# Optimization experiments

Hardware: AMD Instinct MI355X
Metric: run time of the kernel (lower is better)

The kernel has to match this reference:

```python
import jax, jax.numpy as jnp
import numpy as np
from jax import lax

B, S, DIMS, T, K = 4, 4096, 2048, 10, 2


def setup_inputs() -> dict:
    key = jax.random.key(0)
    ks = jax.random.split(key, 4)
    scale = 1.0 / np.sqrt(DIMS)
    x = jax.random.normal(ks[0], (B, S, DIMS), dtype=jnp.float32)
    W_cls = jax.random.normal(ks[1], (DIMS, T), dtype=jnp.float32) * scale
    W_sparse = jax.random.normal(ks[2], (DIMS, T), dtype=jnp.float32) * scale
    W_gates = jax.random.normal(ks[3], (DIMS, T), dtype=jnp.float32) * scale
    return {
        "x": x,
        "W_cls": W_cls, "b_cls": jnp.zeros((T,), jnp.float32),
        "W_sparse": W_sparse, "b_sparse": jnp.zeros((T,), jnp.float32),
        "W_gates": W_gates, "b_gates": jnp.zeros((T,), jnp.float32),
        "alpha": jnp.ones((1,), jnp.float32),
    }


def reference(x, W_cls, b_cls, W_sparse, b_sparse, W_gates, b_gates, alpha):
    # soft routing: softmax classifier over num_types
    soft_types = jax.nn.softmax(jnp.einsum("bsd,dt->bst", x, W_cls) + b_cls, axis=-1)
    # sparse routing: top-k over logits, softmax over the k kept logits,
    # scattered back into a dense [B,S,T] gate vector (zeros elsewhere)
    logits = jnp.einsum("bsd,dt->bst", x, W_sparse) + b_sparse
    top_v, top_i = lax.top_k(logits, K)                      # [B,S,K]
    sparse_g = jax.nn.softmax(top_v, axis=-1)                # [B,S,K]
    # scatter via one-hot (K and T are tiny)
    sparse_types = jnp.sum(jax.nn.one_hot(top_i, T, dtype=x.dtype) * sparse_g[..., None], axis=-2)  # [B,S,T]
    # per-type sigmoid gates: batched single matmul == stack of Linear(dims,1)+Sigmoid
    gates = jax.nn.sigmoid(jnp.einsum("bsd,dt->bst", x, W_gates) + b_gates)  # [B,S,T]
    a = jax.nn.sigmoid(alpha)                                # [1], broadcasts
    mixed_types = a * sparse_types + (1.0 - a) * soft_types  # [B,S,T]
    # original: gates stacked as [B,S,1,T], mixed unsqueezed to [B,S,1,T], sum over T -> [B,S,1]
    return jnp.sum(gates * mixed_types, axis=-1, keepdims=True)
```

## Files before the change

### kernel.cpp

```cpp
#include <hip/hip_runtime.h>
#include <math.h>
#include <stdint.h>


#define NROWS   16384
#define DIMS_   2048
#define TT      10

typedef __attribute__((ext_vector_type(8))) short short8;
typedef __attribute__((ext_vector_type(4))) float f32x4;

__device__ __forceinline__ unsigned short bf16_rne(float f) {
    unsigned int u = __float_as_uint(f);
    unsigned int r = u + 0x7fffu + ((u >> 16) & 1u);
    return (unsigned short)(r >> 16);
}

__global__ __launch_bounds__(256)
void tgate_k0(const float* __restrict__ W_cls,
              const float* __restrict__ W_sparse,
              const float* __restrict__ W_gates,
              unsigned short* __restrict__ frag)
{
    int t = blockIdx.x * 256 + threadIdx.x;
    int K0   = t >> 7;
    int nt   = (t >> 6) & 1;
    int lane = t & 63;
    int n  = nt * 16 + (lane & 15);
    int kb = K0 * 32 + (lane >> 4) * 8;
    short8 hi, lo;
    #pragma unroll
    for (int j = 0; j < 8; ++j) {
        int k = kb + j;
        float w = 0.0f;
        if (n < 10)      w = W_cls[k * TT + n];
        else if (n < 20) w = W_sparse[k * TT + n - 10];
        else if (n < 30) w = W_gates[k * TT + n - 20];
        unsigned short h = bf16_rne(w);
        float back = __uint_as_float(((unsigned int)h) << 16);
        hi[j] = (short)h;
        lo[j] = (short)bf16_rne(w - back);
    }
    short8* fv = reinterpret_cast<short8*>(frag);
    fv[(K0 * 4 + nt * 2 + 0) * 64 + lane] = hi;
    fv[(K0 * 4 + nt * 2 + 1) * 64 + lane] = lo;
}

__device__ __forceinline__ void stage_span(const float* __restrict__ x,
                                           float* buf, int row0, int lane,
                                           int colf0)
{
    #pragma unroll
    for (int r = 0; r < 16; ++r) {
        const float* gp = x + (size_t)(row0 + r) * DIMS_ + colf0 + lane * 4;
        __builtin_amdgcn_global_load_lds(
            (const __attribute__((address_space(1))) void*)gp,
            (__attribute__((address_space(3))) void*)(buf + r * 260),
            16, 0, 0);
    }
}

__global__ __launch_bounds__(256)
void tgate_k1(const float* __restrict__ x,
              const unsigned short* __restrict__ frag,
              const float* __restrict__ b_cls,
              const float* __restrict__ b_sparse,
              const float* __restrict__ b_gates,
              const float* __restrict__ alpha,
              float* __restrict__ out)
{
    __shared__ alignas(16) float smem[4 * 4160];

    const int tid   = threadIdx.x;
    const int lane  = tid & 63;
    const int wv    = __builtin_amdgcn_readfirstlane(tid >> 6);
    const int row0  = blockIdx.x * 16;
    const int m     = lane & 15;
    const int quad  = lane >> 4;
    const int cbase = wv * 512;

    float* buf = smem + wv * 4160;
    const short8* fv    = reinterpret_cast<const short8*>(frag);
    const short8* fbase = fv + (16 * wv * 4) * 64 + lane;

    f32x4 acc[2][2];
    #pragma unroll
    for (int h = 0; h < 2; ++h) {
        acc[h][0] = (f32x4){0.f, 0.f, 0.f, 0.f};
        acc[h][1] = (f32x4){0.f, 0.f, 0.f, 0.f};
    }

    stage_span(x, buf, row0, lane, cbase);
    __builtin_amdgcn_sched_barrier(0);

    short8 F[2][4];
    #pragma unroll
    for (int p = 0; p < 2; ++p) {
        #pragma unroll
        for (int j = 0; j < 4; ++j)
            F[p][j] = fbase[(p * 4 + j) * 64];
    }
    __builtin_amdgcn_sched_barrier(0);

    __builtin_amdgcn_s_waitcnt(0x0F78);
    __builtin_amdgcn_sched_barrier(0);

    #pragma unroll
    for (int k = 0; k < 16; ++k) {
        if (k == 8) {
            __builtin_amdgcn_s_waitcnt(0xC07F);
            __builtin_amdgcn_sched_barrier(0);
            stage_span(x, buf, row0, lane, cbase + 256);
            __builtin_amdgcn_s_waitcnt(0x0F70);
            __builtin_amdgcn_sched_barrier(0);
        }
        const int h = k >> 3;
        const float* src = buf + m * 260 + (k & 7) * 32 + quad * 8;
        float4 b0 = *reinterpret_cast<const float4*>(src);
        float4 b1 = *reinterpret_cast<const float4*>(src + 4);
        float f[8] = {b0.x, b0.y, b0.z, b0.w, b1.x, b1.y, b1.z, b1.w};
        short8 ah, al;
        #pragma unroll
        for (int j = 0; j < 8; ++j) {
            unsigned short hh = bf16_rne(f[j]);
            float back = __uint_as_float(((unsigned int)hh) << 16);
            ah[j] = (short)hh;
            al[j] = (short)bf16_rne(f[j] - back);
        }
        short8 h0 = F[k & 1][0], l0 = F[k & 1][1];
        short8 h1 = F[k & 1][2], l1 = F[k & 1][3];

        acc[h][0] = __builtin_amdgcn_mfma_f32_16x16x32_bf16(ah, h0, acc[h][0], 0, 0, 0);
        acc[h][0] = __builtin_amdgcn_mfma_f32_16x16x32_bf16(al, h0, acc[h][0], 0, 0, 0);
        acc[h][0] = __builtin_amdgcn_mfma_f32_16x16x32_bf16(ah, l0, acc[h][0], 0, 0, 0);
        acc[h][1] = __builtin_amdgcn_mfma_f32_16x16x32_bf16(ah, h1, acc[h][1], 0, 0, 0);
        acc[h][1] = __builtin_amdgcn_mfma_f32_16x16x32_bf16(al, h1, acc[h][1], 0, 0, 0);
        acc[h][1] = __builtin_amdgcn_mfma_f32_16x16x32_bf16(ah, l1, acc[h][1], 0, 0, 0);

        if (k + 2 < 16) {
            #pragma unroll
            for (int j = 0; j < 4; ++j)
                F[k & 1][j] = fbase[((k + 2) * 4 + j) * 64];
        }
    }

    float* red = smem;
    __syncthreads();
    #pragma unroll
    for (int h = 0; h < 2; ++h) {
        int s = 2 * wv + h;
        #pragma unroll
        for (int r = 0; r < 4; ++r) {
            int row = quad * 4 + r;
            red[(s * 16 + row) * 33 + m]      = acc[h][0][r];
            red[(s * 16 + row) * 33 + m + 16] = acc[h][1][r];
        }
    }
    __syncthreads();

    float* fold = red + 8 * 16 * 33;
    #pragma unroll
    for (int u = 0; u < 2; ++u) {
        int i = tid * 2 + u;
        int row = i >> 5, j = i & 31;
        float a = 0.0f;
        #pragma unroll
        for (int s = 0; s < 8; ++s) a += red[(s * 16 + row) * 33 + j];
        fold[row * 33 + j] = a;
    }
    __syncthreads();

    if (tid < 16) {
        const float* l = &fold[tid * 33];
        float lc[TT], lsp[TT], g[TT];
        #pragma unroll
        for (int t = 0; t < TT; ++t) {
            lc[t]  = l[t]      + b_cls[t];
            lsp[t] = l[10 + t] + b_sparse[t];
            float lg = l[20 + t] + b_gates[t];
            g[t] = 1.0f / (1.0f + __expf(-lg));
        }
        float mm = lc[0];
        #pragma unroll
        for (int t = 1; t < TT; ++t) mm = fmaxf(mm, lc[t]);
        float esum = 0.0f, gdot = 0.0f;
        #pragma unroll
        for (int t = 0; t < TT; ++t) {
            float e = __expf(lc[t] - mm);
            esum += e;
            gdot = fmaf(g[t], e, gdot);
        }
        float v1 = lsp[0], v2 = -1e30f, gv1 = g[0], gv2 = 0.0f;
        #pragma unroll
        for (int t = 1; t < TT; ++t) {
            if (lsp[t] > v1)      { v2 = v1; gv2 = gv1; v1 = lsp[t]; gv1 = g[t]; }
            else if (lsp[t] > v2) { v2 = lsp[t]; gv2 = g[t]; }
        }
        float s1 = 1.0f / (1.0f + __expf(v2 - v1));
        float s2 = 1.0f - s1;
        float a  = 1.0f / (1.0f + __expf(-alpha[0]));
        float sparse_dot = fmaf(gv1, s1, gv2 * s2);
        out[row0 + tid] = fmaf(a, sparse_dot, (1.0f - a) * (gdot / esum));
    }
}

extern "C" void kernel_launch(void* const* d_in, const int* in_sizes, int n_in,
                              void* d_out, int out_size, void* d_ws, size_t ws_size,
                              hipStream_t stream) {
    const float* x        = (const float*)d_in[0];
    const float* W_cls    = (const float*)d_in[1];
    const float* b_cls    = (const float*)d_in[2];
    const float* W_sparse = (const float*)d_in[3];
    const float* b_sparse = (const float*)d_in[4];
    const float* W_gates  = (const float*)d_in[5];
    const float* b_gates  = (const float*)d_in[6];
    const float* alpha    = (const float*)d_in[7];
    float* out = (float*)d_out;

    unsigned short* frag = (unsigned short*)d_ws;

    tgate_k0<<<dim3(32), dim3(256), 0, stream>>>(W_cls, W_sparse, W_gates, frag);
    tgate_k1<<<dim3(NROWS / 16), dim3(256), 0, stream>>>(x, frag, b_cls, b_sparse,
                                                         b_gates, alpha, out);
}
```

Baseline: 209.8 us.

## Pipeline x staging into four rotating LDS chunks with fine-grained waitcnts

Replaces the two-phase 16-row span staging (load half, wait, compute, load second half) with four 64-column chunk buffers per wave. Each chunk is consumed by a pair of k-steps and then refilled with the next chunk, with per-step vmcnt waits. This is meant to overlap global-to-LDS loads with MFMA compute instead of stalling halfway through. It relies on hand-coded waitcnt encodings being correct, which adds a correctness risk.

```diff
diff --git a/kernel.cpp b/kernel.cpp
--- a/kernel.cpp
+++ b/kernel.cpp
@@ -6,6 +6,14 @@
 #define NROWS   16384
 #define DIMS_   2048
 #define TT      10
+
+#define WV12  0x0F7C
+#define WV20  0x4F74
+#define WV24  0x4F78
+#define WV28  0x4F7C
+#define WV32  0x8F70
+#define WV36  0x8F74
+#define WLGKM0 0xC07F
 
 typedef __attribute__((ext_vector_type(8))) short short8;
 typedef __attribute__((ext_vector_type(4))) float f32x4;
@@ -46,17 +54,58 @@
     fv[(K0 * 4 + nt * 2 + 1) * 64 + lane] = lo;
 }
 
-__device__ __forceinline__ void stage_span(const float* __restrict__ x,
-                                           float* buf, int row0, int lane,
-                                           int colf0)
-{
-    #pragma unroll
-    for (int r = 0; r < 16; ++r) {
-        const float* gp = x + (size_t)(row0 + r) * DIMS_ + colf0 + lane * 4;
+__device__ __forceinline__ void issue_chunk(const float* __restrict__ x,
+                                            float* bufbase, int row0, int lane,
+                                            int colf0)
+{
+    #pragma unroll
+    for (int t = 0; t < 4; ++t) {
+        const float* gp = x + (size_t)(row0 + 4 * t + (lane >> 4)) * DIMS_
+                            + colf0 + (lane & 15) * 4;
         __builtin_amdgcn_global_load_lds(
             (const __attribute__((address_space(1))) void*)gp,
-            (__attribute__((address_space(3))) void*)(buf + r * 260),
+            (__attribute__((address_space(3))) void*)(bufbase + t * 260),
             16, 0, 0);
+    }
+}
+
+template<int C>
+__device__ __forceinline__ void step_pair(const float* Lbuf,
+                                          const short8* fbase,
+                                          int m, int quad,
+                                          f32x4 (&acc)[2][2],
+                                          short8 (&F)[2][4])
+{
+    #pragma unroll
+    for (int u = 0; u < 2; ++u) {
+        const int k = 2 * C + u;
+        const int h = k >> 3;
+        const float* src = Lbuf + (m >> 2) * 260 + (m & 3) * 64 + u * 32 + quad * 8;
+        float4 b0 = *reinterpret_cast<const float4*>(src);
+        float4 b1 = *reinterpret_cast<const float4*>(src + 4);
+        float f[8] = {b0.x, b0.y, b0.z, b0.w, b1.x, b1.y, b1.z, b1.w};
+        short8 ah, al;
+        #pragma unroll
+        for (int j = 0; j < 8; ++j) {
+            unsigned short hh = bf16_rne(f[j]);
+            float back = __uint_as_float(((unsigned int)hh) << 16);
+            ah[j] = (short)hh;
+            al[j] = (short)bf16_rne(f[j] - back);
+        }
+        short8 h0 = F[u][0], l0 = F[u][1], h1 = F[u][2], l1 = F[u][3];
+
+        acc[h][0] = __builtin_amdgcn_mfma_f32_16x16x32_bf16(ah, h0, acc[h][0], 0, 0, 0);
+        acc[h][0] = __builtin_amdgcn_mfma_f32_16x16x32_bf16(al, h0, acc[h][0], 0, 0, 0);
+        acc[h][0] = __builtin_amdgcn_mfma_f32_16x16x32_bf16(ah, l0, acc[h][0], 0, 0, 0);
+        acc[h][1] = __builtin_amdgcn_mfma_f32_16x16x32_bf16(ah, h1, acc[h][1], 0, 0, 0);
+        acc[h][1] = __builtin_amdgcn_mfma_f32_16x16x32_bf16(al, h1, acc[h][1], 0, 0, 0);
+        acc[h][1] = __builtin_amdgcn_mfma_f32_16x16x32_bf16(ah, l1, acc[h][1], 0, 0, 0);
+
+        if (k + 2 < 16) {
+            #pragma unroll
+            for (int j = 0; j < 4; ++j)
+                F[u][j] = fbase[((k + 2) * 4 + j) * 64];
+        }
     }
 }
 
@@ -79,7 +128,7 @@
     const int quad  = lane >> 4;
     const int cbase = wv * 512;
 
-    float* buf = smem + wv * 4160;
+    float* bufs = smem + wv * 4160;
     const short8* fv    = reinterpret_cast<const short8*>(frag);
     const short8* fbase = fv + (16 * wv * 4) * 64 + lane;
 
@@ -90,9 +139,6 @@
         acc[h][1] = (f32x4){0.f, 0.f, 0.f, 0.f};
     }
 
-    stage_span(x, buf, row0, lane, cbase);
-    __builtin_amdgcn_sched_barrier(0);
-
     short8 F[2][4];
     #pragma unroll
     for (int p = 0; p < 2; ++p) {
@@ -101,48 +147,36 @@
             F[p][j] = fbase[(p * 4 + j) * 64];
     }
     __builtin_amdgcn_sched_barrier(0);
-
-    __builtin_amdgcn_s_waitcnt(0x0F78);
+    issue_chunk(x, bufs + 0 * 1040, row0, lane, cbase + 0 * 64);
+    issue_chunk(x, bufs + 1 * 1040, row0, lane, cbase + 1 * 64);
+    issue_chunk(x, bufs + 2 * 1040, row0, lane, cbase + 2 * 64);
+    issue_chunk(x, bufs + 3 * 1040, row0, lane, cbase + 3 * 64);
     __builtin_amdgcn_sched_barrier(0);
 
-    #pragma unroll
-    for (int k = 0; k < 16; ++k) {
-        if (k == 8) {
-            __builtin_amdgcn_s_waitcnt(0xC07F);
-            __builtin_amdgcn_sched_barrier(0);
-            stage_span(x, buf, row0, lane, cbase + 256);
-            __builtin_amdgcn_s_waitcnt(0x0F70);
-            __builtin_amdgcn_sched_barrier(0);
-        }
-        const int h = k >> 3;
-        const float* src = buf + m * 260 + (k & 7) * 32 + quad * 8;
-        float4 b0 = *reinterpret_cast<const float4*>(src);
-        float4 b1 = *reinterpret_cast<const float4*>(src + 4);
-        float f[8] = {b0.x, b0.y, b0.z, b0.w, b1.x, b1.y, b1.z, b1.w};
-        short8 ah, al;
-        #pragma unroll
-        for (int j = 0; j < 8; ++j) {
-            unsigned short hh = bf16_rne(f[j]);
-            float back = __uint_as_float(((unsigned int)hh) << 16);
-            ah[j] = (short)hh;
-            al[j] = (short)bf16_rne(f[j] - back);
-        }
-        short8 h0 = F[k & 1][0], l0 = F[k & 1][1];
-        short8 h1 = F[k & 1][2], l1 = F[k & 1][3];
-
-        acc[h][0] = __builtin_amdgcn_mfma_f32_16x16x32_bf16(ah, h0, acc[h][0], 0, 0, 0);
-        acc[h][0] = __builtin_amdgcn_mfma_f32_16x16x32_bf16(al, h0, acc[h][0], 0, 0, 0);
-        acc[h][0] = __builtin_amdgcn_mfma_f32_16x16x32_bf16(ah, l0, acc[h][0], 0, 0, 0);
-        acc[h][1] = __builtin_amdgcn_mfma_f32_16x16x32_bf16(ah, h1, acc[h][1], 0, 0, 0);
-        acc[h][1] = __builtin_amdgcn_mfma_f32_16x16x32_bf16(al, h1, acc[h][1], 0, 0, 0);
-        acc[h][1] = __builtin_amdgcn_mfma_f32_16x16x32_bf16(ah, l1, acc[h][1], 0, 0, 0);
-
-        if (k + 2 < 16) {
-            #pragma unroll
-            for (int j = 0; j < 4; ++j)
-                F[k & 1][j] = fbase[((k + 2) * 4 + j) * 64];
-        }
-    }
+    #define KITER(c, WCODE, DO_STAGE)                                        \
+    {                                                                        \
+        __builtin_amdgcn_s_waitcnt(WCODE);                                   \
+        __builtin_amdgcn_sched_barrier(0);                                   \
+        step_pair<c>(bufs + ((c) & 3) * 1040, fbase, m, quad, acc, F);       \
+        __builtin_amdgcn_sched_barrier(0);                                   \
+        if (DO_STAGE) {                                                      \
+            __builtin_amdgcn_s_waitcnt(WLGKM0);                              \
+            __builtin_amdgcn_sched_barrier(0);                               \
+            issue_chunk(x, bufs + ((c) & 3) * 1040, row0, lane,              \
+                        cbase + ((c) + 4) * 64);                             \
+            __builtin_amdgcn_sched_barrier(0);                               \
+        }                                                                    \
+    }
+
+    KITER(0, WV12, 1)
+    KITER(1, WV20, 1)
+    KITER(2, WV28, 1)
+    KITER(3, WV36, 1)
+    KITER(4, WV36, 0)
+    KITER(5, WV32, 0)
+    KITER(6, WV28, 0)
+    KITER(7, WV24, 0)
+    #undef KITER
 
     float* red = smem;
     __syncthreads();
```

After: 210.9 us. No clear change (+0.6%).

## Split K across 16 waves per block with all loads issued upfront

Applied to the files above, without the earlier changes.

Each block now runs 1024 threads (16 waves), and each wave handles a 128-column K slice instead of 512. Every wave issues both of its x chunks and all of its weight fragments at the start, then waits on the chunks one after the other, which removes the mid-loop restaging. The aim is more memory-level parallelism and more loads in flight to hide latency on this bandwidth-bound read of x. The cost is a larger cross-wave reduction across 16 partial sums in LDS and more barrier overhead per block.

```diff
diff --git a/kernel.cpp b/kernel.cpp
--- a/kernel.cpp
+++ b/kernel.cpp
@@ -46,21 +46,22 @@
     fv[(K0 * 4 + nt * 2 + 1) * 64 + lane] = lo;
 }
 
-__device__ __forceinline__ void stage_span(const float* __restrict__ x,
-                                           float* buf, int row0, int lane,
-                                           int colf0)
+__device__ __forceinline__ void issue_chunk(const float* __restrict__ x,
+                                            float* bufbase, int row0, int lane,
+                                            int colf0)
 {
     #pragma unroll
-    for (int r = 0; r < 16; ++r) {
-        const float* gp = x + (size_t)(row0 + r) * DIMS_ + colf0 + lane * 4;
+    for (int t = 0; t < 4; ++t) {
+        const float* gp = x + (size_t)(row0 + 4 * t + (lane >> 4)) * DIMS_
+                            + colf0 + (lane & 15) * 4;
         __builtin_amdgcn_global_load_lds(
             (const __attribute__((address_space(1))) void*)gp,
-            (__attribute__((address_space(3))) void*)(buf + r * 260),
+            (__attribute__((address_space(3))) void*)(bufbase + t * 260),
             16, 0, 0);
     }
 }
 
-__global__ __launch_bounds__(256)
+__global__ __launch_bounds__(1024, 4)
 void tgate_k1(const float* __restrict__ x,
               const unsigned short* __restrict__ frag,
               const float* __restrict__ b_cls,
@@ -69,7 +70,7 @@
               const float* __restrict__ alpha,
               float* __restrict__ out)
 {
-    __shared__ alignas(16) float smem[4 * 4160];
+    __shared__ alignas(16) float smem[16 * 2080];
 
     const int tid   = threadIdx.x;
     const int lane  = tid & 63;
@@ -77,96 +78,85 @@
     const int row0  = blockIdx.x * 16;
     const int m     = lane & 15;
     const int quad  = lane >> 4;
-    const int cbase = wv * 512;
-
-    float* buf = smem + wv * 4160;
+    const int cbase = wv * 128;
+
+    float* bufs = smem + wv * 2080;
     const short8* fv    = reinterpret_cast<const short8*>(frag);
-    const short8* fbase = fv + (16 * wv * 4) * 64 + lane;
-
-    f32x4 acc[2][2];
-    #pragma unroll
-    for (int h = 0; h < 2; ++h) {
-        acc[h][0] = (f32x4){0.f, 0.f, 0.f, 0.f};
-        acc[h][1] = (f32x4){0.f, 0.f, 0.f, 0.f};
-    }
-
-    stage_span(x, buf, row0, lane, cbase);
-    __builtin_amdgcn_sched_barrier(0);
-
-    short8 F[2][4];
-    #pragma unroll
-    for (int p = 0; p < 2; ++p) {
+    const short8* fbase = fv + (4 * wv * 4) * 64 + lane;
+
+    f32x4 accA = (f32x4){0.f, 0.f, 0.f, 0.f};
+    f32x4 accB = (f32x4){0.f, 0.f, 0.f, 0.f};
+
+    short8 F[4][4];
+    #pragma unroll
+    for (int p = 0; p < 4; ++p) {
         #pragma unroll
         for (int j = 0; j < 4; ++j)
             F[p][j] = fbase[(p * 4 + j) * 64];
     }
     __builtin_amdgcn_sched_barrier(0);
-
-    __builtin_amdgcn_s_waitcnt(0x0F78);
+    issue_chunk(x, bufs,        row0, lane, cbase);
+    issue_chunk(x, bufs + 1040, row0, lane, cbase + 64);
     __builtin_amdgcn_sched_barrier(0);
 
-    #pragma unroll
-    for (int k = 0; k < 16; ++k) {
-        if (k == 8) {
-            __builtin_amdgcn_s_waitcnt(0xC07F);
-            __builtin_amdgcn_sched_barrier(0);
-            stage_span(x, buf, row0, lane, cbase + 256);
+    __builtin_amdgcn_s_waitcnt(0x0F74);
+    __builtin_amdgcn_sched_barrier(0);
+
+    #pragma unroll
+    for (int c = 0; c < 2; ++c) {
+        if (c == 1) {
             __builtin_amdgcn_s_waitcnt(0x0F70);
             __builtin_amdgcn_sched_barrier(0);
         }
-        const int h = k >> 3;
-        const float* src = buf + m * 260 + (k & 7) * 32 + quad * 8;
-        float4 b0 = *reinterpret_cast<const float4*>(src);
-        float4 b1 = *reinterpret_cast<const float4*>(src + 4);
-        float f[8] = {b0.x, b0.y, b0.z, b0.w, b1.x, b1.y, b1.z, b1.w};
-        short8 ah, al;
-        #pragma unroll
-        for (int j = 0; j < 8; ++j) {
-            unsigned short hh = bf16_rne(f[j]);
-            float back = __uint_as_float(((unsigned int)hh) << 16);
-            ah[j] = (short)hh;
-            al[j] = (short)bf16_rne(f[j] - back);
-        }
-        short8 h0 = F[k & 1][0], l0 = F[k & 1][1];
-        short8 h1 = F[k & 1][2], l1 = F[k & 1][3];
-
-        acc[h][0] = __builtin_amdgcn_mfma_f32_16x16x32_bf16(ah, h0, acc[h][0], 0, 0, 0);
-        acc[h][0] = __builtin_amdgcn_mfma_f32_16x16x32_bf16(al, h0, acc[h][0], 0, 0, 0);
-        acc[h][0] = __builtin_amdgcn_mfma_f32_16x16x32_bf16(ah, l0, acc[h][0], 0, 0, 0);
-        acc[h][1] = __builtin_amdgcn_mfma_f32_16x16x32_bf16(ah, h1, acc[h][1], 0, 0, 0);
-        acc[h][1] = __builtin_amdgcn_mfma_f32_16x16x32_bf16(al, h1, acc[h][1], 0, 0, 0);
-        acc[h][1] = __builtin_amdgcn_mfma_f32_16x16x32_bf16(ah, l1, acc[h][1], 0, 0, 0);
-
-        if (k + 2 < 16) {
+        const float* Lbuf = bufs + c * 1040;
+        #pragma unroll
+        for (int u = 0; u < 2; ++u) {
+            const int p = 2 * c + u;
+            const float* src = Lbuf + (m >> 2) * 260 + (m & 3) * 64
+                                    + u * 32 + quad * 8;
+            float4 b0 = *reinterpret_cast<const float4*>(src);
+            float4 b1 = *reinterpret_cast<const float4*>(src + 4);
+            float f[8] = {b0.x, b0.y, b0.z, b0.w, b1.x, b1.y, b1.z, b1.w};
+            short8 ah, al;
             #pragma unroll
-            for (int j = 0; j < 4; ++j)
-                F[k & 1][j] = fbase[((k + 2) * 4 + j) * 64];
+            for (int j = 0; j < 8; ++j) {
+                unsigned short hh = bf16_rne(f[j]);
+                float back = __uint_as_float(((unsigned int)hh) << 16);
+                ah[j] = (short)hh;
+                al[j] = (short)bf16_rne(f[j] - back);
+            }
+            short8 h0 = F[p][0], l0 = F[p][1], h1 = F[p][2], l1 = F[p][3];
+
+            accA = __builtin_amdgcn_mfma_f32_16x16x32_bf16(ah, h0, accA, 0, 0, 0);
+            accA = __builtin_amdgcn_mfma_f32_16x16x32_bf16(al, h0, accA, 0, 0, 0);
+            accA = __builtin_amdgcn_mfma_f32_16x16x32_bf16(ah, l0, accA, 0, 0, 0);
+            accB = __builtin_amdgcn_mfma_f32_16x16x32_bf16(ah, h1, accB, 0, 0, 0);
+            accB = __builtin_amdgcn_mfma_f32_16x16x32_bf16(al, h1, accB, 0, 0, 0);
+            accB = __builtin_amdgcn_mfma_f32_16x16x32_bf16(ah, l1, accB, 0, 0, 0);
         }
     }
 
     float* red = smem;
     __syncthreads();
     #pragma unroll
-    for (int h = 0; h < 2; ++h) {
-        int s = 2 * wv + h;
-        #pragma unroll
-        for (int r = 0; r < 4; ++r) {
-            int row = quad * 4 + r;
-            red[(s * 16 + row) * 33 + m]      = acc[h][0][r];
-            red[(s * 16 + row) * 33 + m + 16] = acc[h][1][r];
-        }
+    for (int r = 0; r < 4; ++r) {
+        int row = quad * 4 + r;
+        red[(wv * 16 + row) * 33 + m]      = accA[r];
+        red[(wv * 16 + row) * 33 + m + 16] = accB[r];
     }
     __syncthreads();
 
-    float* fold = red + 8 * 16 * 33;
-    #pragma unroll
-    for (int u = 0; u < 2; ++u) {
-        int i = tid * 2 + u;
-        int row = i >> 5, j = i & 31;
-        float a = 0.0f;
-        #pragma unroll
-        for (int s = 0; s < 8; ++s) a += red[(s * 16 + row) * 33 + j];
-        fold[row * 33 + j] = a;
+    float* fold = red + 16 * 16 * 33;
+    if (tid < 256) {
+        #pragma unroll
+        for (int u = 0; u < 2; ++u) {
+            int i = tid * 2 + u;
+            int row = i >> 5, j = i & 31;
+            float a = 0.0f;
+            #pragma unroll
+            for (int s = 0; s < 16; ++s) a += red[(s * 16 + row) * 33 + j];
+            fold[row * 33 + j] = a;
+        }
     }
     __syncthreads();
 
@@ -220,6 +210,6 @@
     unsigned short* frag = (unsigned short*)d_ws;
 
     tgate_k0<<<dim3(32), dim3(256), 0, stream>>>(W_cls, W_sparse, W_gates, frag);
-    tgate_k1<<<dim3(NROWS / 16), dim3(256), 0, stream>>>(x, frag, b_cls, b_sparse,
-                                                         b_gates, alpha, out);
-}
+    tgate_k1<<<dim3(NROWS / 16), dim3(1024), 0, stream>>>(x, frag, b_cls, b_sparse,
+                                                          b_gates, alpha, out);
+}
```

Result: no change. 212.8 us (+1.4%).
